# Kernel tuning notes

Measured on AMD Instinct MI355X. Metric: run time of the kernel, lower is better.

## Reference

```python
import jax, jax.numpy as jnp
import numpy as np
import math

B, T, E = 1, 2048, 2048
H, D = 16, 128
L = 64
RA_WINDOW = 64
RA_ALPHA = 0.5


def setup_inputs() -> dict:
    key = jax.random.key(0)
    ks = jax.random.split(key, 7)
    s_e = 1.0 / math.sqrt(E)
    s_l = 1.0 / math.sqrt(L)
    return {
        "hidden_states": jax.random.normal(ks[0], (B, T, E), jnp.float32),
        "Wq": jax.random.normal(ks[1], (E, E), jnp.float32) * s_e,       # q_proj.weight [out,in]
        "Wk": jax.random.normal(ks[2], (L, E), jnp.float32) * s_e,       # k_down.weight
        "Wv": jax.random.normal(ks[3], (L, E), jnp.float32) * s_e,       # v_down.weight
        "q_to_latent": jax.random.normal(ks[4], (H, D, L), jnp.float32) * (1.0 / math.sqrt(D)),
        "v_up": jax.random.normal(ks[5], (H, L, D), jnp.float32) * s_l,
        "Wo": jax.random.normal(ks[6], (E, E), jnp.float32) * s_e,       # out_proj.weight
    }


def reference(hidden_states, Wq, Wk, Wv, q_to_latent, v_up, Wo):
    B_, T_, E_ = hidden_states.shape
    NEG = jnp.asarray(-1e30, hidden_states.dtype)

    # per-head queries [B,T,H,D]
    Q = (hidden_states @ Wq.T).reshape(B_, T_, H, D)
    # shared latent K/V [B,T,L]
    latent_k = hidden_states @ Wk.T
    latent_v = hidden_states @ Wv.T

    # per-head Q -> latent alignment [B,T,H,L]
    q_latent = jnp.einsum('bthd,hdl->bthl', Q, q_to_latent)

    inv_sqrt_L = 1.0 / math.sqrt(L)
    # main latent-compressed logits [B,H,T,T]
    logits = jnp.einsum('bthl,bsl->bhts', q_latent, latent_k) * inv_sqrt_L

    i = jnp.arange(T_)[:, None]
    j = jnp.arange(T_)[None, :]
    causal = j <= i                       # [T,T]
    logits = jnp.where(causal[None, None], logits, NEG)

    # reciprocal band pass. NOTE: einsum labels (d vs l) intentionally mismatch,
    # faithfully reproducing the source's outer-product-of-sums computation.
    logits_recip = jnp.einsum('bthd,bsl->bhts', q_latent, latent_k) * inv_sqrt_L
    band = (jnp.abs(i - j) <= RA_WINDOW) & causal
    logits = jnp.where(band[None, None], logits + RA_ALPHA * logits_recip, logits)

    attn = jax.nn.softmax(logits, axis=-1)  # [B,H,T,T]

    # per-head V up-projection [B,T,H,D]
    V_exp = jnp.einsum('btl,hld->bthd', latent_v, v_up)
    ctx = jnp.einsum('bhts,bshd->bthd', attn, V_exp)
    out = ctx.reshape(B_, T_, H * D) @ Wo.T
    return out
```

## Files before the change

kernel.cpp:

```cpp
#include <hip/hip_runtime.h>


#define T_ 2048
#define E_ 2048
#define H_ 16
#define D_ 128
#define L_ 64
#define NQ 1152

typedef float  floatx4 __attribute__((ext_vector_type(4)));
typedef __bf16 bf16x8  __attribute__((ext_vector_type(8)));

__device__ __forceinline__ ushort f2b(float x){
  unsigned int u = __float_as_uint(x);
  u = (u + 0x7fffu + ((u >> 16) & 1u)) >> 16;
  return (ushort)u;
}
__device__ __forceinline__ float blo(unsigned int u){ return __uint_as_float(u << 16); }
__device__ __forceinline__ float bhi(unsigned int u){ return __uint_as_float(u & 0xffff0000u); }

__device__ __forceinline__ void glds16(const ushort* g, ushort* l){
#if __has_builtin(__builtin_amdgcn_global_load_lds)
  __builtin_amdgcn_global_load_lds((const __attribute__((address_space(1))) void*)g,
                                   (__attribute__((address_space(3))) void*)l, 16, 0, 0);
#else
  *(uint4*)l = *(const uint4*)g;
#endif
}

__global__ __launch_bounds__(256)
void k_f2b4(const float* __restrict__ a, ushort* __restrict__ oa,
            const float* __restrict__ b, ushort* __restrict__ ob,
            const float* __restrict__ c, ushort* __restrict__ oc,
            const float* __restrict__ d, ushort* __restrict__ od){
  int bid = blockIdx.x; const float* src; ushort* dst; int base;
  if (bid < 4096){ src=a; dst=oa; base=bid; }
  else if (bid < 8192){ src=b; dst=ob; base=bid-4096; }
  else if (bid < 8320){ src=c; dst=oc; base=bid-8192; }
  else { src=d; dst=od; base=bid-8320; }
  int i = (base*256 + (int)threadIdx.x)*4;
  float4 v = *(const float4*)(src + i);
  ushort4 o; o.x=f2b(v.x); o.y=f2b(v.y); o.z=f2b(v.z); o.w=f2b(v.w);
  *(ushort4*)(dst + i) = o;
}

__global__ __launch_bounds__(128)
void k_prep_wql(const float* __restrict__ Wq, const float* __restrict__ q2l,
                ushort* __restrict__ Wql){
  const int h = blockIdx.z, lh = blockIdx.y;
  const int e = blockIdx.x*128 + threadIdx.x;
  const float* qb = q2l + (size_t)h*D_*L_ + lh*32;
  float acc[32];
  #pragma unroll
  for (int i=0;i<32;++i) acc[i]=0.f;
  for (int d=0; d<128; ++d){
    float wv = Wq[(size_t)(h*128+d)*E_ + e];
    #pragma unroll
    for (int i=0;i<32;++i) acc[i] += wv*qb[(size_t)d*64 + i];
  }
  #pragma unroll
  for (int i=0;i<32;++i) Wql[(size_t)(h*64 + lh*32 + i)*E_ + e] = f2b(acc[i]);
}

__global__ __launch_bounds__(256)
void k_prep_vupT(const float* __restrict__ vup, ushort* __restrict__ vupT){
  const int h = blockIdx.x, tid = threadIdx.x;
  for (int idx = tid; idx < L_*D_; idx += 256){
    int l = idx >> 7, d = idx & 127;
    vupT[(size_t)h*D_*L_ + d*64 + l] = f2b(vup[(size_t)h*L_*D_ + idx]);
  }
}

template<int MT,int NT,bool OB16>
__global__ __launch_bounds__(256)
void gemm_glds2(const ushort* __restrict__ A, const ushort* __restrict__ B,
                float* __restrict__ Cf, ushort* __restrict__ Cb,
                int M, int N, int K, float scale){
  constexpr int BM = 32*MT, BN = 32*NT;
  constexpr int IA = BM/32, IB = BN/32;
  __shared__ ushort As[BM*64];
  __shared__ ushort Bs[BN*64];
  const int tid = threadIdx.x, lane = tid&63, wv = tid>>6;
  const int wm = wv & 1, wn = wv >> 1;
  const int l15 = lane&15, quad = lane>>4;
  const int nbx = (int)gridDim.x, nwg = nbx*(int)gridDim.y;
  int bid = (int)blockIdx.y*nbx + (int)blockIdx.x;
  bid = (bid & 7)*(nwg >> 3) + (bid >> 3);
  const int m0 = (bid / nbx)*BM, n0 = (bid % nbx)*BN;
  const float sc = (n0 < 1024) ? scale : 1.0f;
  floatx4 acc[MT][NT] = {};
  for (int k0=0; k0<K; k0+=64){
    __syncthreads();
    #pragma unroll
    for (int j=0;j<IA;++j){
      int cc = j*256 + tid; int row = cc>>3, kc = ((cc&7)^(row&7))*8;
      glds16(A + (size_t)(m0+row)*K + k0 + kc, &As[cc*8]);
    }
    #pragma unroll
    for (int j=0;j<IB;++j){
      int cc = j*256 + tid; int row = cc>>3, kc = ((cc&7)^(row&7))*8;
      glds16(B + (size_t)(n0+row)*K + k0 + kc, &Bs[cc*8]);
    }
    __syncthreads();
    #pragma unroll
    for (int kk=0;kk<2;++kk){
      bf16x8 af[MT], bfr[NT];
      #pragma unroll
      for (int mi=0;mi<MT;++mi){
        const int r = wm*MT*16 + mi*16 + l15;
        af[mi] = *(const bf16x8*)(&As[r*64 + (((kk*4+quad)^(r&7))<<3)]);
      }
      #pragma unroll
      for (int ni=0;ni<NT;++ni){
        const int r = wn*NT*16 + ni*16 + l15;
        bfr[ni] = *(const bf16x8*)(&Bs[r*64 + (((kk*4+quad)^(r&7))<<3)]);
      }
      #pragma unroll
      for (int mi=0;mi<MT;++mi)
        #pragma unroll
        for (int ni=0;ni<NT;++ni)
          acc[mi][ni] = __builtin_amdgcn_mfma_f32_16x16x32_bf16(af[mi], bfr[ni], acc[mi][ni], 0,0,0);
    }
  }
  #pragma unroll
  for (int mi=0;mi<MT;++mi){
    const int rb = m0 + wm*MT*16 + mi*16 + quad*4;
    #pragma unroll
    for (int ni=0;ni<NT;++ni){
      const int col = n0 + wn*NT*16 + ni*16 + l15;
      #pragma unroll
      for (int r=0;r<4;++r){
        if constexpr (OB16) Cb[(size_t)(rb+r)*N + col] = f2b(acc[mi][ni][r]*sc);
        else                Cf[(size_t)(rb+r)*N + col] = acc[mi][ni][r];
      }
    }
  }
}

__global__ __launch_bounds__(256)
void k_rowsums(const ushort* __restrict__ qkvb,
               float* __restrict__ rsq, float* __restrict__ rsk){
  int i = blockIdx.x*256 + threadIdx.x;
  const ushort* src; float* dst;
  if (i < T_*H_){
    int t = i>>4, g = i&15;
    src = qkvb + (size_t)t*NQ + g*64; dst = rsq + i;
  } else {
    int t = i - T_*H_;
    if (t >= T_) return;
    src = qkvb + (size_t)t*NQ + 1024; dst = rsk + t;
  }
  const uint4* p = (const uint4*)src;
  float s = 0.f;
  #pragma unroll
  for (int j=0;j<8;++j){
    uint4 u = p[j];
    const unsigned int uu[4] = {u.x,u.y,u.z,u.w};
    #pragma unroll
    for (int q=0;q<4;++q){ s += blo(uu[q]); s += bhi(uu[q]); }
  }
  *dst = s;
}

__global__ __launch_bounds__(256)
void k_vexp_mfma(const ushort* __restrict__ qkvb, const ushort* __restrict__ vupT,
                 ushort* __restrict__ vexpT){
  const int h = blockIdx.y, t0 = blockIdx.x*64;
  const int tid = threadIdx.x, lane = tid&63, w = tid>>6;
  const int l15 = lane&15, quad = lane>>4;
  bf16x8 a[2][2], b[4][2];
  #pragma unroll
  for (int mt=0;mt<2;++mt)
    #pragma unroll
    for (int kk=0;kk<2;++kk)
      a[mt][kk] = *(const bf16x8*)(vupT + (size_t)h*D_*L_ + (w*32+mt*16+l15)*64 + kk*32 + quad*8);
  #pragma unroll
  for (int nt=0;nt<4;++nt)
    #pragma unroll
    for (int kk=0;kk<2;++kk)
      b[nt][kk] = *(const bf16x8*)(qkvb + (size_t)(t0+nt*16+l15)*NQ + 1088 + kk*32 + quad*8);
  floatx4 acc[2][4] = {};
  #pragma unroll
  for (int mt=0;mt<2;++mt)
    #pragma unroll
    for (int nt=0;nt<4;++nt)
      #pragma unroll
      for (int kk=0;kk<2;++kk)
        acc[mt][nt] = __builtin_amdgcn_mfma_f32_16x16x32_bf16(a[mt][kk], b[nt][kk], acc[mt][nt], 0,0,0);
  #pragma unroll
  for (int mt=0;mt<2;++mt)
    #pragma unroll
    for (int nt=0;nt<4;++nt)
      #pragma unroll
      for (int r=0;r<4;++r)
        vexpT[((size_t)h*D_ + w*32+mt*16+quad*4+r)*T_ + t0 + nt*16 + l15] = f2b(acc[mt][nt][r]);
}

__global__ __launch_bounds__(256, 2)
void k_attn(const ushort* __restrict__ qkvb,
            const float*  __restrict__ rsq,
            const float*  __restrict__ rsk,
            const ushort* __restrict__ vexpT,
            ushort*       __restrict__ ctx,
            ushort*       __restrict__ partO,
            float*        __restrict__ partML,
            int CH){
  __shared__ ushort Ks[2][64*64];
  __shared__ ushort Vts[2][128*64];
  __shared__ ushort Ps[4*16*64];
  const int h  = blockIdx.y;
  const int bxr = (int)gridDim.x - 1 - (int)blockIdx.x;
  int qt, c;
  if (CH == 8){
    if (bxr < 8){ qt = bxr; c = 0; }
    else if (bxr < 24){ int u = bxr-8;  qt = 8  + (u>>1); c = u&1; }
    else if (bxr < 48){ int u = bxr-24; qt = 16 + u/3;    c = u - (u/3)*3; }
    else               { int u = bxr-48; qt = 24 + (u>>2); c = u&3; }
  } else { qt = bxr; c = 0; }
  const int nct = (qt + CH) / CH;
  const int stBeg = c*CH, stEnd = min(qt, stBeg + CH - 1);
  const int t0 = qt*64;
  const int tid = threadIdx.x, lane = tid & 63, w = tid >> 6;
  const int l15 = lane & 15, quad = lane >> 4;

  auto stageK = [&](int b, int s0k){
    #pragma unroll
    for (int j=0;j<2;++j){ int cc = tid + j*256;
      int row = cc>>3, kc = ((cc&7) ^ (row&7))*8;
      glds16(qkvb + (size_t)(s0k + row)*NQ + 1024 + kc, &Ks[b][cc*8]); }
  };
  auto stageV = [&](int b, int s0v){
    #pragma unroll
    for (int j=0;j<4;++j){ int cc = tid + j*256;
      int row = cc>>3, sc2 = ((cc&7) ^ (row&7))*8;
      glds16(vexpT + ((size_t)h*128 + row)*T_ + s0v + sc2, &Vts[b][cc*8]); }
  };

  const int qrow = t0 + w*16 + l15;
  const bf16x8 q0 = *(const bf16x8*)(qkvb + (size_t)qrow*NQ + h*64 + quad*8);
  const bf16x8 q1 = *(const bf16x8*)(qkvb + (size_t)qrow*NQ + h*64 + 32 + quad*8);
  const float rqv = rsq[(size_t)qrow*H_ + h] * 0.5f;

  float mrun = -INFINITY, lrun = 0.f;
  floatx4 o[8] = {};

  stageK(0, stBeg*64); stageV(0, stBeg*64);

  for (int st=stBeg; st<=stEnd; ++st){
    const int s0 = st*64;
    const int cur = (st - stBeg) & 1;
    const bool more = (st < stEnd);
    const bool edge = (st >= qt-1);
    float4 rk[4];
    if (edge){
      #pragma unroll
      for (int jt=0;jt<4;++jt) rk[jt] = *(const float4*)(rsk + s0 + jt*16 + quad*4);
    }
    if (more){ stageK(cur^1, s0 + 64); stageV(cur^1, s0 + 64); }
    if (more) asm volatile("s_waitcnt vmcnt(6)" ::: "memory");
    else      asm volatile("s_waitcnt vmcnt(0)" ::: "memory");
    __builtin_amdgcn_s_barrier();
    __builtin_amdgcn_sched_barrier(0);
    floatx4 sT[4] = {};
    __builtin_amdgcn_s_setprio(1);
    #pragma unroll
    for (int jt=0;jt<4;++jt){
      const int srow = jt*16 + l15, sx = srow & 7;
      bf16x8 k0f = *(const bf16x8*)(&Ks[cur][srow*64 + (quad^sx)*8]);
      sT[jt] = __builtin_amdgcn_mfma_f32_16x16x32_bf16(k0f, q0, sT[jt], 0,0,0);
      bf16x8 k1f = *(const bf16x8*)(&Ks[cur][srow*64 + ((4+quad)^sx)*8]);
      sT[jt] = __builtin_amdgcn_mfma_f32_16x16x32_bf16(k1f, q1, sT[jt], 0,0,0);
    }
    __builtin_amdgcn_s_setprio(0);
    float mloc = -3.0e38f;
    if (edge){
      #pragma unroll
      for (int jt=0;jt<4;++jt){
        #pragma unroll
        for (int r=0;r<4;++r){
          const int sg = s0 + jt*16 + quad*4 + r;
          const int dd = qrow - sg;
          float x = sT[jt][r];
          x = (dd <= 64) ? x + rqv*((const float*)&rk[jt])[r] : x;
          x = (dd < 0)   ? -3.0e38f : x;
          sT[jt][r] = x; mloc = fmaxf(mloc, x);
        }
      }
    } else {
      #pragma unroll
      for (int jt=0;jt<4;++jt)
        #pragma unroll
        for (int r=0;r<4;++r) mloc = fmaxf(mloc, sT[jt][r]);
    }
    mloc = fmaxf(mloc, __shfl_xor(mloc, 16));
    mloc = fmaxf(mloc, __shfl_xor(mloc, 32));
    const float mn = (mloc - mrun <= 6.0f) ? mrun : mloc;
    const float al = exp2f(mrun - mn);
    float ss = 0.f;
    #pragma unroll
    for (int jt=0;jt<4;++jt)
      #pragma unroll
      for (int r=0;r<4;++r){
        float p = exp2f(sT[jt][r]-mn); sT[jt][r] = p; ss += p;
      }
    ss += __shfl_xor(ss, 16); ss += __shfl_xor(ss, 32);
    lrun = lrun*al + ss; mrun = mn;
    #pragma unroll
    for (int jt=0;jt<4;++jt){
      unsigned p01, p23;
      asm volatile("v_cvt_pk_bf16_f32 %0, %1, %2" : "=v"(p01) : "v"(sT[jt][0]), "v"(sT[jt][1]));
      asm volatile("v_cvt_pk_bf16_f32 %0, %1, %2" : "=v"(p23) : "v"(sT[jt][2]), "v"(sT[jt][3]));
      const int chunk = 2*jt + (quad>>1);
      uint2 pw2; pw2.x = p01; pw2.y = p23;
      *(uint2*)(&Ps[(w*16 + l15)*64 + ((chunk ^ (l15&7))<<3) + (quad&1)*4]) = pw2;
    }
    if (__any(al < 1.0f)){
      float alr[4];
      #pragma unroll
      for (int r=0;r<4;++r) alr[r] = __shfl(al, quad*4 + r);
      #pragma unroll
      for (int nt=0;nt<8;++nt){
        o[nt][0]*=alr[0]; o[nt][1]*=alr[1]; o[nt][2]*=alr[2]; o[nt][3]*=alr[3];
      }
    }
    __builtin_amdgcn_s_setprio(1);
    #pragma unroll
    for (int kks=0;kks<2;++kks){
      const int ch = kks*4 + quad;
      bf16x8 pf = *(const bf16x8*)(&Ps[(w*16 + l15)*64 + ((ch ^ (l15&7))<<3)]);
      #pragma unroll
      for (int nt=0;nt<8;++nt){
        const int vrow = nt*16 + l15, vx = vrow & 7;
        bf16x8 vf = *(const bf16x8*)(&Vts[cur][vrow*64 + ((kks*4+quad)^vx)*8]);
        o[nt] = __builtin_amdgcn_mfma_f32_16x16x32_bf16(pf, vf, o[nt], 0,0,0);
      }
    }
    __builtin_amdgcn_s_setprio(0);
    __builtin_amdgcn_sched_barrier(0);
    if (more) __builtin_amdgcn_s_barrier();
  }
  const float linv = 1.f/lrun;
  float lr4[4];
  #pragma unroll
  for (int r=0;r<4;++r) lr4[r] = __shfl(linv, quad*4 + r);
  if (nct == 1){
    #pragma unroll
    for (int r=0;r<4;++r){
      const int row = t0 + w*16 + quad*4 + r;
      #pragma unroll
      for (int nt=0;nt<8;++nt)
        ctx[(size_t)row*E_ + h*D_ + nt*16 + l15] = f2b(o[nt][r]*lr4[r]);
    }
  } else {
    const int slot = (h*24 + (qt-8))*4 + c;
    ushort* po = partO + (size_t)slot*8192;
    #pragma unroll
    for (int nt=0;nt<8;++nt)
      #pragma unroll
      for (int r=0;r<4;++r)
        po[((w*8+nt)*4+r)*64 + quad*16 + l15] = f2b(o[nt][r]*lr4[r]);
    if (quad == 0){
      float2 ml; ml.x = mrun; ml.y = lrun;
      ((float2*)partML)[(size_t)slot*64 + w*16 + l15] = ml;
    }
  }
}

__global__ __launch_bounds__(256)
void k_merge(const ushort* __restrict__ partO, const float* __restrict__ partML,
             ushort* __restrict__ ctx){
  const int h = blockIdx.y, qt = 8 + blockIdx.x;
  const int nct = (qt + 8) / 8;
  const int tid = threadIdx.x;
  const int rg = tid >> 2, d0 = (tid & 3)*32;
  const int w = rg >> 4, quad = (rg >> 2) & 3, rr = rg & 3;
  const int n0 = d0 >> 4;
  const int sbase = (h*24 + (qt-8))*4;
  float m[4], l[4], M = -INFINITY;
  for (int c=0;c<4;++c){
    if (c < nct){
      float2 v = ((const float2*)partML)[(size_t)(sbase+c)*64 + rg];
      m[c]=v.x; l[c]=v.y; M = fmaxf(M, v.x);
    }
  }
  float lt = 0.f, wgt[4];
  for (int c=0;c<4;++c){
    if (c < nct){ wgt[c] = exp2f(m[c]-M)*l[c]; lt += wgt[c]; }
  }
  const float inv = 1.f/lt;
  float acc[32];
  #pragma unroll
  for (int i=0;i<32;++i) acc[i]=0.f;
  for (int c=0;c<4;++c){
    if (c >= nct) break;
    const float sc = wgt[c]*inv;
    const ushort* po = partO + (size_t)(sbase+c)*8192;
    #pragma unroll
    for (int nn=0;nn<2;++nn){
      const ushort* p2 = po + ((w*8 + n0+nn)*4 + rr)*64 + quad*16;
      uint4 u  = *(const uint4*)p2;
      uint4 u2 = *(const uint4*)(p2 + 8);
      const unsigned int uu[8] = {u.x,u.y,u.z,u.w,u2.x,u2.y,u2.z,u2.w};
      #pragma unroll
      for (int q=0;q<8;++q){
        acc[nn*16+q*2]   += sc*blo(uu[q]);
        acc[nn*16+q*2+1] += sc*bhi(uu[q]);
      }
    }
  }
  ushort* dst = ctx + (size_t)(qt*64 + rg)*E_ + h*D_ + d0;
  #pragma unroll
  for (int k=0;k<8;++k){
    ushort4 ov; ov.x=f2b(acc[k*4]); ov.y=f2b(acc[k*4+1]);
    ov.z=f2b(acc[k*4+2]); ov.w=f2b(acc[k*4+3]);
    *(ushort4*)(dst + k*4) = ov;
  }
}

extern "C" void kernel_launch(void* const* d_in, const int* in_sizes, int n_in,
                              void* d_out, int out_size, void* d_ws, size_t ws_size,
                              hipStream_t stream) {
  const float* hs  = (const float*)d_in[0];
  const float* Wq  = (const float*)d_in[1];
  const float* Wk  = (const float*)d_in[2];
  const float* Wv  = (const float*)d_in[3];
  const float* q2l = (const float*)d_in[4];
  const float* vup = (const float*)d_in[5];
  const float* Wo  = (const float*)d_in[6];
  float* out = (float*)d_out;
  char* ws = (char*)d_ws;

  ushort* hsb   = (ushort*)(ws + 0);
  ushort* Wqkvb = (ushort*)(ws + 8388608);
  ushort* Wob   = (ushort*)(ws + 13107200);
  ushort* qkvb  = (ushort*)(ws + 21495808);
  ushort* vupT  = (ushort*)(ws + 26214400);
  float*  rsqp  = (float*) (ws + 26476544);
  float*  rskp  = (float*) (ws + 26607616);
  ushort* vexpT = (ushort*)(ws + 26615808);
  ushort* ctxb  = (ushort*)(ws + 35004416);
  ushort* partO = (ushort*)(ws + 43393024);
  float*  partML= (float*) (ws + 68558848);
  const size_t NEED = 69345280;
  const int CH = (ws_size >= NEED) ? 8 : 32;

  k_f2b4<<<8448, 256, 0, stream>>>(hs, hsb, Wo, Wob,
                                   Wk, Wqkvb + (size_t)1024*E_,
                                   Wv, Wqkvb + (size_t)1088*E_);

  k_prep_wql<<<dim3(16,2,16), 128, 0, stream>>>(Wq, q2l, Wqkvb);
  k_prep_vupT<<<16, 256, 0, stream>>>(vup, vupT);

  gemm_glds2<2,2,true><<<dim3(18,32), 256, 0, stream>>>(
      hsb, Wqkvb, nullptr, qkvb, T_, NQ, E_, 0.18033688f);

  k_rowsums<<<136, 256, 0, stream>>>(qkvb, rsqp, rskp);

  k_vexp_mfma<<<dim3(32,16), 256, 0, stream>>>(qkvb, vupT, vexpT);

  k_attn<<<dim3(CH==8 ? 80 : 32, 16), 256, 0, stream>>>(
      qkvb, rsqp, rskp, vexpT, ctxb, partO, partML, CH);

  if (CH == 8)
    k_merge<<<dim3(24,16), 256, 0, stream>>>(partO, partML, ctxb);

  gemm_glds2<2,4,false><<<dim3(16,32), 256, 0, stream>>>(
      ctxb, Wob, out, nullptr, T_, E_, E_, 1.0f);
}
```

Before: 257.0 us.

## Split attention blocks into single-wave workgroups loading K/V directly from global

Each 256-thread attention workgroup becomes four 64-thread workgroups, one per 16-row query slice, with the grid scaled by four. The shared-memory double-buffered staging of K and V via global-to-LDS loads and the associated barriers are removed; each wave now loads its K and V fragments straight from global memory into registers. This removes block-level synchronisation and LDS staging cost but loses K/V reuse across the four waves, quadrupling global/L2 traffic for K and V and exposing load latency without explicit prefetch.

```diff
diff --git a/kernel.cpp b/kernel.cpp
--- a/kernel.cpp
+++ b/kernel.cpp
@@ -196,7 +196,7 @@
         vexpT[((size_t)h*D_ + w*32+mt*16+quad*4+r)*T_ + t0 + nt*16 + l15] = f2b(acc[mt][nt][r]);
 }
 
-__global__ __launch_bounds__(256, 2)
+__global__ __launch_bounds__(64)
 void k_attn(const ushort* __restrict__ qkvb,
             const float*  __restrict__ rsq,
             const float*  __restrict__ rsk,
@@ -205,73 +205,65 @@
             ushort*       __restrict__ partO,
             float*        __restrict__ partML,
             int CH){
-  __shared__ ushort Ks[2][64*64];
-  __shared__ ushort Vts[2][128*64];
-  __shared__ ushort Ps[4*16*64];
+  __shared__ ushort Ps[16*64];
   const int h  = blockIdx.y;
   const int bxr = (int)gridDim.x - 1 - (int)blockIdx.x;
+  const int outer = bxr >> 2, w = bxr & 3;
   int qt, c;
   if (CH == 8){
-    if (bxr < 8){ qt = bxr; c = 0; }
-    else if (bxr < 24){ int u = bxr-8;  qt = 8  + (u>>1); c = u&1; }
-    else if (bxr < 48){ int u = bxr-24; qt = 16 + u/3;    c = u - (u/3)*3; }
-    else               { int u = bxr-48; qt = 24 + (u>>2); c = u&3; }
-  } else { qt = bxr; c = 0; }
+    if (outer < 8){ qt = outer; c = 0; }
+    else if (outer < 24){ int u = outer-8;  qt = 8  + (u>>1); c = u&1; }
+    else if (outer < 48){ int u = outer-24; qt = 16 + u/3;    c = u - (u/3)*3; }
+    else                { int u = outer-48; qt = 24 + (u>>2); c = u&3; }
+  } else { qt = outer; c = 0; }
   const int nct = (qt + CH) / CH;
   const int stBeg = c*CH, stEnd = min(qt, stBeg + CH - 1);
   const int t0 = qt*64;
-  const int tid = threadIdx.x, lane = tid & 63, w = tid >> 6;
+  const int lane = threadIdx.x;
   const int l15 = lane & 15, quad = lane >> 4;
-
-  auto stageK = [&](int b, int s0k){
-    #pragma unroll
-    for (int j=0;j<2;++j){ int cc = tid + j*256;
-      int row = cc>>3, kc = ((cc&7) ^ (row&7))*8;
-      glds16(qkvb + (size_t)(s0k + row)*NQ + 1024 + kc, &Ks[b][cc*8]); }
-  };
-  auto stageV = [&](int b, int s0v){
-    #pragma unroll
-    for (int j=0;j<4;++j){ int cc = tid + j*256;
-      int row = cc>>3, sc2 = ((cc&7) ^ (row&7))*8;
-      glds16(vexpT + ((size_t)h*128 + row)*T_ + s0v + sc2, &Vts[b][cc*8]); }
-  };
 
   const int qrow = t0 + w*16 + l15;
   const bf16x8 q0 = *(const bf16x8*)(qkvb + (size_t)qrow*NQ + h*64 + quad*8);
   const bf16x8 q1 = *(const bf16x8*)(qkvb + (size_t)qrow*NQ + h*64 + 32 + quad*8);
   const float rqv = rsq[(size_t)qrow*H_ + h] * 0.5f;
 
+  const ushort* vbase = vexpT + (size_t)h*D_*T_;
+
   float mrun = -INFINITY, lrun = 0.f;
   floatx4 o[8] = {};
 
-  stageK(0, stBeg*64); stageV(0, stBeg*64);
-
   for (int st=stBeg; st<=stEnd; ++st){
     const int s0 = st*64;
-    const int cur = (st - stBeg) & 1;
-    const bool more = (st < stEnd);
     const bool edge = (st >= qt-1);
     float4 rk[4];
     if (edge){
       #pragma unroll
       for (int jt=0;jt<4;++jt) rk[jt] = *(const float4*)(rsk + s0 + jt*16 + quad*4);
     }
-    if (more){ stageK(cur^1, s0 + 64); stageV(cur^1, s0 + 64); }
-    if (more) asm volatile("s_waitcnt vmcnt(6)" ::: "memory");
-    else      asm volatile("s_waitcnt vmcnt(0)" ::: "memory");
-    __builtin_amdgcn_s_barrier();
-    __builtin_amdgcn_sched_barrier(0);
+    const ushort* kb = qkvb + (size_t)s0*NQ + 1024;
+    bf16x8 k0[4], k1[4];
+    #pragma unroll
+    for (int jt=0;jt<4;++jt){
+      const int srow = jt*16 + l15;
+      k0[jt] = *(const bf16x8*)(kb + (size_t)srow*NQ + quad*8);
+      k1[jt] = *(const bf16x8*)(kb + (size_t)srow*NQ + 32 + quad*8);
+    }
+    bf16x8 vf0[8];
+    #pragma unroll
+    for (int nt=0;nt<8;++nt)
+      vf0[nt] = *(const bf16x8*)(vbase + (size_t)(nt*16+l15)*T_ + s0 + quad*8);
     floatx4 sT[4] = {};
     __builtin_amdgcn_s_setprio(1);
     #pragma unroll
     for (int jt=0;jt<4;++jt){
-      const int srow = jt*16 + l15, sx = srow & 7;
-      bf16x8 k0f = *(const bf16x8*)(&Ks[cur][srow*64 + (quad^sx)*8]);
-      sT[jt] = __builtin_amdgcn_mfma_f32_16x16x32_bf16(k0f, q0, sT[jt], 0,0,0);
-      bf16x8 k1f = *(const bf16x8*)(&Ks[cur][srow*64 + ((4+quad)^sx)*8]);
-      sT[jt] = __builtin_amdgcn_mfma_f32_16x16x32_bf16(k1f, q1, sT[jt], 0,0,0);
+      sT[jt] = __builtin_amdgcn_mfma_f32_16x16x32_bf16(k0[jt], q0, sT[jt], 0,0,0);
+      sT[jt] = __builtin_amdgcn_mfma_f32_16x16x32_bf16(k1[jt], q1, sT[jt], 0,0,0);
     }
     __builtin_amdgcn_s_setprio(0);
+    bf16x8 vf1[8];
+    #pragma unroll
+    for (int nt=0;nt<8;++nt)
+      vf1[nt] = *(const bf16x8*)(vbase + (size_t)(nt*16+l15)*T_ + s0 + 32 + quad*8);
     float mloc = -3.0e38f;
     if (edge){
       #pragma unroll
@@ -312,7 +304,7 @@
       asm volatile("v_cvt_pk_bf16_f32 %0, %1, %2" : "=v"(p23) : "v"(sT[jt][2]), "v"(sT[jt][3]));
       const int chunk = 2*jt + (quad>>1);
       uint2 pw2; pw2.x = p01; pw2.y = p23;
-      *(uint2*)(&Ps[(w*16 + l15)*64 + ((chunk ^ (l15&7))<<3) + (quad&1)*4]) = pw2;
+      *(uint2*)(&Ps[l15*64 + ((chunk ^ (l15&7))<<3) + (quad&1)*4]) = pw2;
     }
     if (__any(al < 1.0f)){
       float alr[4];
@@ -324,20 +316,17 @@
       }
     }
     __builtin_amdgcn_s_setprio(1);
-    #pragma unroll
-    for (int kks=0;kks<2;++kks){
-      const int ch = kks*4 + quad;
-      bf16x8 pf = *(const bf16x8*)(&Ps[(w*16 + l15)*64 + ((ch ^ (l15&7))<<3)]);
-      #pragma unroll
-      for (int nt=0;nt<8;++nt){
-        const int vrow = nt*16 + l15, vx = vrow & 7;
-        bf16x8 vf = *(const bf16x8*)(&Vts[cur][vrow*64 + ((kks*4+quad)^vx)*8]);
-        o[nt] = __builtin_amdgcn_mfma_f32_16x16x32_bf16(pf, vf, o[nt], 0,0,0);
-      }
+    {
+      bf16x8 pf0 = *(const bf16x8*)(&Ps[l15*64 + ((quad ^ (l15&7))<<3)]);
+      #pragma unroll
+      for (int nt=0;nt<8;++nt)
+        o[nt] = __builtin_amdgcn_mfma_f32_16x16x32_bf16(pf0, vf0[nt], o[nt], 0,0,0);
+      bf16x8 pf1 = *(const bf16x8*)(&Ps[l15*64 + (((4+quad) ^ (l15&7))<<3)]);
+      #pragma unroll
+      for (int nt=0;nt<8;++nt)
+        o[nt] = __builtin_amdgcn_mfma_f32_16x16x32_bf16(pf1, vf1[nt], o[nt], 0,0,0);
     }
     __builtin_amdgcn_s_setprio(0);
-    __builtin_amdgcn_sched_barrier(0);
-    if (more) __builtin_amdgcn_s_barrier();
   }
   const float linv = 1.f/lrun;
   float lr4[4];
@@ -458,7 +447,7 @@
 
   k_vexp_mfma<<<dim3(32,16), 256, 0, stream>>>(qkvb, vupT, vexpT);
 
-  k_attn<<<dim3(CH==8 ? 80 : 32, 16), 256, 0, stream>>>(
+  k_attn<<<dim3(CH==8 ? 320 : 128, 16), 64, 0, stream>>>(
       qkvb, rsqp, rskp, vexpT, ctxb, partO, partML, CH);
 
   if (CH == 8)
```

After: 323.9 us. 26.0% more time.
